# Kernel tuning notes

Measured on AMD Instinct MI355X. Metric: run time of the kernel, lower is better.

## Reference

```python
import jax, jax.numpy as jnp
import numpy as np

B, S, HID = 2, 2048, 2560
H, HKV, D = 8, 4, 256          # query heads, kv heads, head_dim
GROUPS = H // HKV
Q_SIZE, KV_SIZE = H * D, HKV * D
SLIDING_WINDOW = 512
SCALE = 256.0 ** -0.5          # query_pre_attn_scalar ** -0.5
EPS = 1e-6
ROPE_THETA = 10000.0


def setup_inputs() -> dict:
    key = jax.random.key(0)
    k1, k2, k3 = jax.random.split(key, 3)
    return {
        "hidden_states": jax.random.normal(k1, (B, S, HID), jnp.float32),
        "w_qkv": jax.random.normal(k2, (HID, Q_SIZE + 2 * KV_SIZE), jnp.float32) * (HID ** -0.5),
        "w_o": jax.random.normal(k3, (H * D, HID), jnp.float32) * ((H * D) ** -0.5),
        "q_norm_w": jnp.zeros((D,), jnp.float32),   # Gemma RMSNorm uses (1 + w)
        "k_norm_w": jnp.zeros((D,), jnp.float32),
        "positions": jnp.arange(S, dtype=jnp.int32),
    }


def _gemma_rms_norm(x, w, eps=EPS):
    # Gemma3RMSNorm: normalize in fp32, scale by (1 + w)
    xf = x.astype(jnp.float32)
    n = xf * jax.lax.rsqrt(jnp.mean(xf * xf, axis=-1, keepdims=True) + eps)
    return (n * (1.0 + w)).astype(x.dtype)


def _rope(q, k, positions):
    # q: [B,S,H,D], k: [B,S,HKV,D]; rotate_half RoPE, unsqueeze_dim=2 (head axis)
    half = D // 2
    inv_freq = 1.0 / (ROPE_THETA ** (jnp.arange(0, D, 2, dtype=jnp.float32) / D))  # [D/2]
    ang = positions.astype(jnp.float32)[:, None] * inv_freq[None, :]               # [S,D/2]
    emb = jnp.concatenate([ang, ang], axis=-1)                                     # [S,D]
    cos = jnp.cos(emb)[None, :, None, :]
    sin = jnp.sin(emb)[None, :, None, :]

    def rot(x):
        x1, x2 = x[..., :half], x[..., half:]
        return jnp.concatenate([-x2, x1], axis=-1)

    return q * cos + rot(q) * sin, k * cos + rot(k) * sin


def reference(hidden_states, w_qkv, w_o, q_norm_w, k_norm_w, positions):
    bsz, q_len, _ = hidden_states.shape
    qkv = jnp.einsum("bsh,hd->bsd", hidden_states, w_qkv)
    q, k, v = jnp.split(qkv, [Q_SIZE, Q_SIZE + KV_SIZE], axis=-1)
    Q = q.reshape(bsz, q_len, H, D)
    K = k.reshape(bsz, q_len, HKV, D)
    V = v.reshape(bsz, q_len, HKV, D)

    Q = _gemma_rms_norm(Q, q_norm_w)
    K = _gemma_rms_norm(K, k_norm_w)
    Q, K = _rope(Q, K, positions)

    # GQA: repeat kv heads to match query heads
    Kr = jnp.repeat(K, GROUPS, axis=2)  # [B,S,H,D]
    Vr = jnp.repeat(V, GROUPS, axis=2)

    scores = jnp.einsum("bqhd,bkhd->bhqk", Q, Kr) * SCALE  # [B,H,S,S]

    i = positions[:, None].astype(jnp.int32)
    j = positions[None, :].astype(jnp.int32)
    mask = (j <= i) & ((i - j) < SLIDING_WINDOW)           # causal + sliding window
    scores = jnp.where(mask[None, None, :, :], scores, jnp.float32(-1e30))

    probs = jax.nn.softmax(scores.astype(jnp.float32), axis=-1).astype(Q.dtype)
    out = jnp.einsum("bhqk,bkhd->bqhd", probs, Vr).reshape(bsz, q_len, H * D)
    return jnp.einsum("bsd,dh->bsh", out, w_o)
```

## Files before the change

### kernel.cpp

```cpp
#include <hip/hip_runtime.h>
#include <hip/hip_bf16.h>
#include <stdint.h>

#define QSCALE 0.09016844005555459f

typedef __attribute__((ext_vector_type(4))) float f32x4;
typedef __attribute__((ext_vector_type(8))) __bf16 bf16x8;
typedef __attribute__((ext_vector_type(8))) unsigned short ushort8;

static __device__ __forceinline__ float bf2f(unsigned short v) {
  union { unsigned u; float f; } x; x.u = ((unsigned)v) << 16; return x.f;
}
static __device__ __forceinline__ unsigned short f2bf(float f) {
  union { float f; unsigned u; } x; x.f = f;
  unsigned r = x.u + 0x7fffu + ((x.u >> 16) & 1u);
  return (unsigned short)(r >> 16);
}
static __device__ __forceinline__ void gload16(const void* g, void* l) {
  __builtin_amdgcn_global_load_lds((const __attribute__((address_space(1))) void*)g,
                                   (__attribute__((address_space(3))) void*)l, 16, 0, 0);
}
#define SBAR() __builtin_amdgcn_s_barrier()

__global__ __launch_bounds__(256) void k_rope_tab(const int* __restrict__ pos,
                                                  float* __restrict__ ct,
                                                  float* __restrict__ st) {
  int idx = blockIdx.x * 256 + threadIdx.x;
  int s = idx >> 7, j = idx & 127;
  float inv = exp2f((float)j * (-13.287712379549449f / 128.0f));
  float ang = (float)pos[s] * inv;
  float sv, cv;
  sincosf(ang, &sv, &cv);
  ct[idx] = cv; st[idx] = sv;
}

__global__ __launch_bounds__(256) void k_cvt_bf16(const float* __restrict__ in,
                                                  unsigned short* __restrict__ out, int n4) {
  int i = blockIdx.x * 256 + threadIdx.x;
  if (i >= n4) return;
  float4 v = ((const float4*)in)[i];
  ushort4 o; o.x = f2bf(v.x); o.y = f2bf(v.y); o.z = f2bf(v.z); o.w = f2bf(v.w);
  ((ushort4*)out)[i] = o;
}

__global__ __launch_bounds__(256) void k_transpose_w(const float* __restrict__ in,
                                                     unsigned short* __restrict__ out,
                                                     int R, int C) {
  __shared__ float tile[32][33];
  int c0 = blockIdx.x * 32, r0 = blockIdx.y * 32;
  int tx = threadIdx.x & 31, ty = threadIdx.x >> 5;
#pragma unroll
  for (int i = 0; i < 4; i++)
    tile[ty + 8*i][tx] = in[(size_t)(r0 + ty + 8*i) * C + c0 + tx];
  __syncthreads();
#pragma unroll
  for (int i = 0; i < 4; i++)
    out[(size_t)(c0 + ty + 8*i) * R + r0 + tx] = f2bf(tile[tx][ty + 8*i]);
}

template <bool F32OUT>
__global__ __launch_bounds__(512, 1) void k_gemm256(const unsigned short* __restrict__ A,
                                                    const unsigned short* __restrict__ Bt,
                                                    void* __restrict__ Cm,
                                                    int M, int N, int K) {
  __shared__ __align__(16) unsigned short ldsA[4][8192];
  __shared__ __align__(16) unsigned short ldsB[4][8192];
  const int nbn = N >> 8;
  int bid = blockIdx.x;
  int nwg = gridDim.x;
  if ((nwg & 7) == 0) {
    int cpx = nwg >> 3;
    bid = (bid & 7) * cpx + (bid >> 3);
  }
  const int bm = bid / nbn, bn = bid % nbn;
  const int tid = threadIdx.x;
  const int w = tid >> 6, l = tid & 63;
  const int wm = w >> 2, wn = w & 3;
  const int lr = l & 15, lk = l >> 4;
  const int nt = K >> 5;

  const int rL = tid >> 2;
  const int swc = ((tid & 3) ^ ((tid >> 3) & 3)) << 3;
  const unsigned short* Ag = A + (size_t)(bm * 256 + rL) * K + swc;
  const unsigned short* Bg = Bt + (size_t)(bn * 256 + rL) * K + swc;
  const int ldsoff = w * 512;
  const int wb = ((lk ^ ((lr >> 1) & 3)) << 3);
  const int arow0 = wm * 128 + lr;
  const int brow0 = wn * 64 + lr;

  f32x4 acc[8][4] = {};

#define STAGE_A(kt_, s_) do { \
    gload16(Ag + (size_t)(kt_) * 32,                    (char*)&ldsA[s_][ldsoff]); \
    gload16(Ag + (size_t)(kt_) * 32 + (size_t)128 * K,  (char*)&ldsA[s_][4096 + ldsoff]); } while (0)
#define STAGE_B(kt_, s_) do { \
    gload16(Bg + (size_t)(kt_) * 32,                    (char*)&ldsB[s_][ldsoff]); \
    gload16(Bg + (size_t)(kt_) * 32 + (size_t)128 * K,  (char*)&ldsB[s_][4096 + ldsoff]); } while (0)

#define KSTEP(kt_, S_, PF_, VMC_, TAILBAR_) do { \
    bf16x8 af[8], bf[4]; \
    _Pragma("unroll") \
    for (int i = 0; i < 8; ++i) \
      af[i] = *(const bf16x8*)&ldsA[S_][((arow0 + i * 16) << 5) + wb]; \
    _Pragma("unroll") \
    for (int j = 0; j < 4; ++j) \
      bf[j] = *(const bf16x8*)&ldsB[S_][((brow0 + j * 16) << 5) + wb]; \
    if (PF_) { STAGE_A((kt_) + 3, ((S_) + 3) & 3); STAGE_B((kt_) + 3, ((S_) + 3) & 3); } \
    __builtin_amdgcn_s_setprio(1); \
    _Pragma("unroll") \
    for (int i = 0; i < 8; ++i) \
      _Pragma("unroll") \
      for (int j = 0; j < 4; ++j) \
        acc[i][j] = __builtin_amdgcn_mfma_f32_16x16x32_bf16(af[i], bf[j], acc[i][j], 0, 0, 0); \
    __builtin_amdgcn_s_setprio(0); \
    if ((VMC_) == 8)      { asm volatile("s_waitcnt vmcnt(8)" ::: "memory"); } \
    else if ((VMC_) == 4) { asm volatile("s_waitcnt vmcnt(4)" ::: "memory"); } \
    else if ((VMC_) == 0) { asm volatile("s_waitcnt vmcnt(0)" ::: "memory"); } \
    if (TAILBAR_) SBAR(); \
  } while (0)

  STAGE_A(0, 0); STAGE_B(0, 0);
  STAGE_A(1, 1); STAGE_B(1, 1);
  STAGE_A(2, 2); STAGE_B(2, 2);
  asm volatile("s_waitcnt vmcnt(8)" ::: "memory");
  SBAR();

  const int ng = nt >> 2;
  for (int g = 0; g < ng - 1; ++g) {
    const int kt0 = g << 2;
    KSTEP(kt0 + 0, 0, true, 8, true);
    KSTEP(kt0 + 1, 1, true, 8, true);
    KSTEP(kt0 + 2, 2, true, 8, true);
    KSTEP(kt0 + 3, 3, true, 8, true);
  }
  {
    const int kt0 = nt - 4;
    KSTEP(kt0 + 0, 0, true, 8, true);
    KSTEP(kt0 + 1, 1, false, 4, true);
    KSTEP(kt0 + 2, 2, false, 0, true);
    KSTEP(kt0 + 3, 3, false, -1, false);
  }
#undef KSTEP
#undef STAGE_A
#undef STAGE_B

#pragma unroll
  for (int i = 0; i < 8; ++i)
#pragma unroll
    for (int j = 0; j < 4; ++j) {
      int row = bm * 256 + wm * 128 + i * 16 + lk * 4;
      int col = bn * 256 + wn * 64 + j * 16 + lr;
#pragma unroll
      for (int r = 0; r < 4; ++r) {
        if constexpr (F32OUT)
          ((float*)Cm)[(size_t)(row + r) * N + col] = acc[i][j][r];
        else
          ((unsigned short*)Cm)[(size_t)(row + r) * N + col] = f2bf(acc[i][j][r]);
      }
    }
}

__global__ __launch_bounds__(256) void k_norm_rope(
    const unsigned short* __restrict__ qkv,
    const float* __restrict__ qw, const float* __restrict__ kw,
    const float* __restrict__ ct, const float* __restrict__ st,
    unsigned short* __restrict__ Qh, unsigned short* __restrict__ Kh) {
  int gwid = (blockIdx.x * 256 + threadIdx.x) >> 6;
  int l = threadIdx.x & 63;
  int head = gwid % 12;
  int bs = gwid / 12;
  int b = bs >> 11, s = bs & 2047;
  bool isq = head < 8;
  int col = isq ? head * 256 : 2048 + (head - 8) * 256;
  const unsigned short* src = qkv + (size_t)bs * 4096 + col;
  int d0 = l * 4;
  ushort4 u = *(const ushort4*)(src + d0);
  float x0 = bf2f(u.x), x1 = bf2f(u.y), x2 = bf2f(u.z), x3 = bf2f(u.w);
  float ss = x0 * x0 + x1 * x1 + x2 * x2 + x3 * x3;
#pragma unroll
  for (int off = 32; off > 0; off >>= 1) ss += __shfl_xor(ss, off);
  float inv = rsqrtf(ss * (1.0f / 256.0f) + 1e-6f);
  const float* wv = isq ? qw : kw;
  float4 w4 = *(const float4*)(wv + d0);
  float y0 = x0 * inv * (1.0f + w4.x);
  float y1 = x1 * inv * (1.0f + w4.y);
  float y2 = x2 * inv * (1.0f + w4.z);
  float y3 = x3 * inv * (1.0f + w4.w);
  int fb = (l & 31) * 4;
  float4 c4 = *(const float4*)(ct + s * 128 + fb);
  float4 s4 = *(const float4*)(st + s * 128 + fb);
  float p0 = __shfl_xor(y0, 32), p1 = __shfl_xor(y1, 32);
  float p2 = __shfl_xor(y2, 32), p3 = __shfl_xor(y3, 32);
  float sg = (l < 32) ? -1.0f : 1.0f;
  float o0 = y0 * c4.x + sg * p0 * s4.x;
  float o1 = y1 * c4.y + sg * p1 * s4.y;
  float o2 = y2 * c4.z + sg * p2 * s4.z;
  float o3 = y3 * c4.w + sg * p3 * s4.w;
  if (isq) {
    o0 *= QSCALE; o1 *= QSCALE; o2 *= QSCALE; o3 *= QSCALE;
    unsigned short* dst = Qh + (((size_t)(b * 8 + head)) * 2048 + s) * 256 + d0;
    ushort4 o; o.x = f2bf(o0); o.y = f2bf(o1); o.z = f2bf(o2); o.w = f2bf(o3);
    *(ushort4*)dst = o;
  } else {
    int hk = head - 8;
    int ch = d0 >> 3;
    int dsw = ((ch ^ (s & 7)) << 3) | (d0 & 7);
    unsigned short* dst = Kh + (((size_t)(b * 4 + hk)) * 2048 + s) * 256 + dsw;
    ushort4 o; o.x = f2bf(o0); o.y = f2bf(o1); o.z = f2bf(o2); o.w = f2bf(o3);
    *(ushort4*)dst = o;
  }
}

__global__ __launch_bounds__(256) void k_vtrans(const unsigned short* __restrict__ qkv,
                                                unsigned short* __restrict__ VT) {
  __shared__ __align__(16) unsigned short tile[64][72];
  int bid = blockIdx.x;
  int dt = bid & 3, stile = (bid >> 2) & 31, hk = (bid >> 7) & 3, b = bid >> 9;
  int s0 = stile * 64, d0 = dt * 64;
  int t = threadIdx.x;
#pragma unroll
  for (int i = 0; i < 2; i++) {
    int flat = i * 256 + t;
    int sl = flat >> 3, dc = flat & 7;
    ushort8 v = *(const ushort8*)&qkv[(size_t)(b * 2048 + s0 + sl) * 4096 + 3072 + hk * 256 + d0 + dc * 8];
    *(ushort8*)&tile[sl][dc * 8] = v;
  }
  __syncthreads();
#pragma unroll
  for (int i = 0; i < 2; i++) {
    int flat = i * 256 + t;
    int dl = flat >> 3, sc = flat & 7;
    ushort8 v;
#pragma unroll
    for (int j = 0; j < 8; j++) v[j] = tile[sc * 8 + j][dl];
    int dg = d0 + dl;
    int chg = (s0 >> 3) + sc;
    int swc = chg ^ (dg & 7);
    *(ushort8*)&VT[((size_t)(b * 4 + hk) * 256 + dg) * 2048 + swc * 8] = v;
  }
}

__global__ __launch_bounds__(512) void k_attn(
    const unsigned short* __restrict__ Qh,
    const unsigned short* __restrict__ Kh,
    const unsigned short* __restrict__ VT,
    const int* __restrict__ pos,
    unsigned short* __restrict__ Ao) {
  __shared__ __align__(16) unsigned short Ks[2][64 * 256];
  __shared__ __align__(16) unsigned short Vs[2][256 * 64];
  __shared__ __align__(16) unsigned short Ps[8][16 * 72];
  int bid = blockIdx.x;
  int qt = bid & 31, hk = (bid >> 5) & 3, b = bid >> 7;
  int t = threadIdx.x, w = t >> 6, l = t & 63;
  int lr = l & 15, lk = l >> 4;
  int h = hk * 2 + (w >> 2);
  int q0 = qt * 64, qrow0 = q0 + (w & 3) * 16;
  const unsigned short* qbase = Qh + (((size_t)(b * 8 + h)) * 2048 + (qrow0 + lr)) * 256;
  bf16x8 qf[8];
#pragma unroll
  for (int c = 0; c < 8; c++) qf[c] = *(const bf16x8*)&qbase[c * 32 + lk * 8];
  int pq[4];
#pragma unroll
  for (int r = 0; r < 4; r++) pq[r] = pos[qrow0 + lk * 4 + r];
  float m[4], ll[4];
  f32x4 oacc[16];
  f32x4 zero4 = {0.f, 0.f, 0.f, 0.f};
#pragma unroll
  for (int r = 0; r < 4; r++) { m[r] = -1e30f; ll[r] = 0.0f; }
#pragma unroll
  for (int nd = 0; nd < 16; nd++) oacc[nd] = zero4;
  const char* Kbase = (const char*)(Kh + ((size_t)(b * 4 + hk)) * 2048 * 256);
  const char* Vbase = (const char*)(VT + ((size_t)(b * 4 + hk)) * 256 * 2048);
  int jlo = q0 - 511; if (jlo < 0) jlo = 0; jlo &= ~63;
  const int ntj = ((q0 + 64) - jlo) >> 6;

#define ASTAGE(tj_) do { \
    const int j0_ = jlo + (tj_) * 64; \
    char* kd_ = (char*)Ks[(tj_) & 1]; \
    char* vd_ = (char*)Vs[(tj_) & 1]; \
    _Pragma("unroll") \
    for (int i = 0; i < 4; i++) \
      gload16(Kbase + (size_t)j0_ * 512 + i * 8192 + t * 16, kd_ + i * 8192 + w * 1024); \
    _Pragma("unroll") \
    for (int i = 0; i < 4; i++) { \
      int off_ = i * 8192 + t * 16; \
      int d_ = off_ >> 7, rb_ = off_ & 127; \
      gload16(Vbase + (size_t)d_ * 4096 + j0_ * 2 + rb_, vd_ + i * 8192 + w * 1024); \
    } \
  } while (0)

  ASTAGE(0);
  for (int tj = 0; tj < ntj; ++tj) {
    const int j0 = jlo + tj * 64;
    const char* Kb = (const char*)Ks[tj & 1];
    const char* Vb = (const char*)Vs[tj & 1];
    if (tj + 1 < ntj) {
      ASTAGE(tj + 1);
      asm volatile("s_waitcnt vmcnt(8)" ::: "memory");
    } else {
      asm volatile("s_waitcnt vmcnt(0)" ::: "memory");
    }
    SBAR();
    f32x4 sacc[4];
#pragma unroll
    for (int n = 0; n < 4; n++) sacc[n] = zero4;
    __builtin_amdgcn_s_setprio(1);
#pragma unroll
    for (int n = 0; n < 4; n++) {
      int key = n * 16 + lr;
      int sw = (key & 7) << 4;
#pragma unroll
      for (int c = 0; c < 8; c++) {
        bf16x8 kf = *(const bf16x8*)(Kb + key * 512 + ((c * 64 + lk * 16) ^ sw));
        sacc[n] = __builtin_amdgcn_mfma_f32_16x16x32_bf16(qf[c], kf, sacc[n], 0, 0, 0);
      }
    }
    __builtin_amdgcn_s_setprio(0);
    int pk[4];
#pragma unroll
    for (int n = 0; n < 4; n++) pk[n] = pos[j0 + n * 16 + lr];
#pragma unroll
    for (int n = 0; n < 4; n++)
#pragma unroll
      for (int r = 0; r < 4; r++) {
        int dq = pq[r] - pk[n];
        if (!(dq >= 0 && dq < 512)) sacc[n][r] = -1e30f;
      }
    float tm[4], rs[4], mn[4], corr[4];
#pragma unroll
    for (int r = 0; r < 4; r++)
      tm[r] = fmaxf(fmaxf(sacc[0][r], sacc[1][r]), fmaxf(sacc[2][r], sacc[3][r]));
#pragma unroll
    for (int d = 1; d < 16; d <<= 1)
#pragma unroll
      for (int r = 0; r < 4; r++) tm[r] = fmaxf(tm[r], __shfl_xor(tm[r], d));
#pragma unroll
    for (int r = 0; r < 4; r++) {
      mn[r] = fmaxf(m[r], tm[r]);
      corr[r] = exp2f(m[r] - mn[r]);
      rs[r] = 0.f;
    }
#pragma unroll
    for (int n = 0; n < 4; n++)
#pragma unroll
      for (int r = 0; r < 4; r++) {
        float sv = sacc[n][r];
        float p = (sv > -1e29f) ? exp2f(sv - mn[r]) : 0.0f;
        sacc[n][r] = p;
        rs[r] += p;
      }
#pragma unroll
    for (int d = 1; d < 16; d <<= 1)
#pragma unroll
      for (int r = 0; r < 4; r++) rs[r] += __shfl_xor(rs[r], d);
#pragma unroll
    for (int r = 0; r < 4; r++) { ll[r] = ll[r] * corr[r] + rs[r]; m[r] = mn[r]; }
#pragma unroll
    for (int nd = 0; nd < 16; nd++)
#pragma unroll
      for (int r = 0; r < 4; r++) oacc[nd][r] *= corr[r];
#pragma unroll
    for (int n = 0; n < 4; n++)
#pragma unroll
      for (int r = 0; r < 4; r++)
        Ps[w][(lk * 4 + r) * 72 + n * 16 + lr] = f2bf(sacc[n][r]);
#pragma unroll
    for (int c2 = 0; c2 < 2; c2++) {
      bf16x8 pf = *(const bf16x8*)&Ps[w][lr * 72 + c2 * 32 + lk * 8];
      __builtin_amdgcn_s_setprio(1);
#pragma unroll
      for (int nd = 0; nd < 16; nd++) {
        int dr = nd * 16 + lr;
        bf16x8 vf = *(const bf16x8*)(Vb + dr * 128 + ((c2 * 64 + lk * 16) ^ ((dr & 7) << 4)));
        oacc[nd] = __builtin_amdgcn_mfma_f32_16x16x32_bf16(pf, vf, oacc[nd], 0, 0, 0);
      }
      __builtin_amdgcn_s_setprio(0);
    }
    SBAR();
  }
#undef ASTAGE
#pragma unroll
  for (int r = 0; r < 4; r++) ll[r] = 1.0f / ll[r];
#pragma unroll
  for (int nd = 0; nd < 16; nd++)
#pragma unroll
    for (int r = 0; r < 4; r++) {
      float v = oacc[nd][r] * ll[r];
      Ao[((size_t)(b * 2048 + qrow0 + lk * 4 + r)) * 2048 + h * 256 + nd * 16 + lr] = f2bf(v);
    }
}

extern "C" void kernel_launch(void* const* d_in, const int* in_sizes, int n_in,
                              void* d_out, int out_size, void* d_ws, size_t ws_size,
                              hipStream_t stream) {
  const float* hs   = (const float*)d_in[0];
  const float* wqkv = (const float*)d_in[1];
  const float* wo   = (const float*)d_in[2];
  const float* qnw  = (const float*)d_in[3];
  const float* knw  = (const float*)d_in[4];
  const int*   pos  = (const int*)d_in[5];
  float* out = (float*)d_out;

  char* base = (char*)d_ws;
  const size_t OFF_R0 = 0;
  const size_t OFF_R1 = 33554432;
  const size_t OFF_R2 = 54525952;
  const size_t OFF_R3 = 75497472;

  unsigned short* QKV = (unsigned short*)(base + OFF_R0);
  unsigned short* Ao  = (unsigned short*)(base + OFF_R0);
  unsigned short* WoT = (unsigned short*)(base + OFF_R0 + 16777216);
  unsigned short* Xb  = (unsigned short*)(base + OFF_R1);
  unsigned short* Qh  = (unsigned short*)(base + OFF_R1);
  unsigned short* WqT = (unsigned short*)(base + OFF_R2);
  unsigned short* Kh  = (unsigned short*)(base + OFF_R2);
  unsigned short* VT  = (unsigned short*)(base + OFF_R2 + 8388608);
  float* ct = (float*)(base + OFF_R3);
  float* st = (float*)(base + OFF_R3 + 1048576);

  k_rope_tab<<<1024, 256, 0, stream>>>(pos, ct, st);
  k_cvt_bf16<<<10240, 256, 0, stream>>>(hs, Xb, 2621440);
  k_transpose_w<<<dim3(128, 80), 256, 0, stream>>>(wqkv, WqT, 2560, 4096);
  k_gemm256<false><<<256, 512, 0, stream>>>(Xb, WqT, QKV, 4096, 4096, 2560);
  k_norm_rope<<<12288, 256, 0, stream>>>(QKV, qnw, knw, ct, st, Qh, Kh);
  k_vtrans<<<1024, 256, 0, stream>>>(QKV, VT);
  k_transpose_w<<<dim3(80, 64), 256, 0, stream>>>(wo, WoT, 2048, 2560);
  k_attn<<<256, 512, 0, stream>>>(Qh, Kh, VT, pos, Ao);
  k_gemm256<true><<<160, 512, 0, stream>>>(Ao, WoT, out, 4096, 2560, 2048);
}
```

Before: 232.4 us.

## Switch GEMM pipeline to double-buffered 64-wide K tiles

Replaces the 4-stage, 32-wide K pipeline in the bf16 GEMM with a 2-stage, 64-wide K tile. Each tile is split into two 32-wide halves, and the next tile is prefetched while the current one is computed. This halves the number of barriers and waitcnt points per K and issues larger load batches. The trade-off is a shallower prefetch distance and a full vmcnt(0) wait every tile, which can expose memory latency. The loop also assumes nt is even.

Result: slower. 247.0 us (+6.3%).

```diff
diff --git a/kernel.cpp b/kernel.cpp
--- a/kernel.cpp
+++ b/kernel.cpp
@@ -63,8 +63,8 @@
                                                     const unsigned short* __restrict__ Bt,
                                                     void* __restrict__ Cm,
                                                     int M, int N, int K) {
-  __shared__ __align__(16) unsigned short ldsA[4][8192];
-  __shared__ __align__(16) unsigned short ldsB[4][8192];
+  __shared__ __align__(16) unsigned short ldsA[2][16384];
+  __shared__ __align__(16) unsigned short ldsB[2][16384];
   const int nbn = N >> 8;
   int bid = blockIdx.x;
   int nwg = gridDim.x;
@@ -77,7 +77,7 @@
   const int w = tid >> 6, l = tid & 63;
   const int wm = w >> 2, wn = w & 3;
   const int lr = l & 15, lk = l >> 4;
-  const int nt = K >> 5;
+  const int nt = K >> 6;
 
   const int rL = tid >> 2;
   const int swc = ((tid & 3) ^ ((tid >> 3) & 3)) << 3;
@@ -90,22 +90,26 @@
 
   f32x4 acc[8][4] = {};
 
-#define STAGE_A(kt_, s_) do { \
-    gload16(Ag + (size_t)(kt_) * 32,                    (char*)&ldsA[s_][ldsoff]); \
-    gload16(Ag + (size_t)(kt_) * 32 + (size_t)128 * K,  (char*)&ldsA[s_][4096 + ldsoff]); } while (0)
-#define STAGE_B(kt_, s_) do { \
-    gload16(Bg + (size_t)(kt_) * 32,                    (char*)&ldsB[s_][ldsoff]); \
-    gload16(Bg + (size_t)(kt_) * 32 + (size_t)128 * K,  (char*)&ldsB[s_][4096 + ldsoff]); } while (0)
-
-#define KSTEP(kt_, S_, PF_, VMC_, TAILBAR_) do { \
+#define STAGE64(kt_, s_) do { \
+    const size_t kb_ = (size_t)(kt_) * 64; \
+    gload16(Ag + kb_,                         (char*)&ldsA[s_][ldsoff]); \
+    gload16(Ag + kb_ + (size_t)128 * K,       (char*)&ldsA[s_][4096 + ldsoff]); \
+    gload16(Ag + kb_ + 32,                    (char*)&ldsA[s_][8192 + ldsoff]); \
+    gload16(Ag + kb_ + 32 + (size_t)128 * K,  (char*)&ldsA[s_][12288 + ldsoff]); \
+    gload16(Bg + kb_,                         (char*)&ldsB[s_][ldsoff]); \
+    gload16(Bg + kb_ + (size_t)128 * K,       (char*)&ldsB[s_][4096 + ldsoff]); \
+    gload16(Bg + kb_ + 32,                    (char*)&ldsB[s_][8192 + ldsoff]); \
+    gload16(Bg + kb_ + 32 + (size_t)128 * K,  (char*)&ldsB[s_][12288 + ldsoff]); \
+  } while (0)
+
+#define HALF64(S_, KH_) do { \
     bf16x8 af[8], bf[4]; \
     _Pragma("unroll") \
     for (int i = 0; i < 8; ++i) \
-      af[i] = *(const bf16x8*)&ldsA[S_][((arow0 + i * 16) << 5) + wb]; \
+      af[i] = *(const bf16x8*)&ldsA[S_][(KH_) * 8192 + ((arow0 + i * 16) << 5) + wb]; \
     _Pragma("unroll") \
     for (int j = 0; j < 4; ++j) \
-      bf[j] = *(const bf16x8*)&ldsB[S_][((brow0 + j * 16) << 5) + wb]; \
-    if (PF_) { STAGE_A((kt_) + 3, ((S_) + 3) & 3); STAGE_B((kt_) + 3, ((S_) + 3) & 3); } \
+      bf[j] = *(const bf16x8*)&ldsB[S_][(KH_) * 8192 + ((brow0 + j * 16) << 5) + wb]; \
     __builtin_amdgcn_s_setprio(1); \
     _Pragma("unroll") \
     for (int i = 0; i < 8; ++i) \
@@ -113,36 +117,26 @@
       for (int j = 0; j < 4; ++j) \
         acc[i][j] = __builtin_amdgcn_mfma_f32_16x16x32_bf16(af[i], bf[j], acc[i][j], 0, 0, 0); \
     __builtin_amdgcn_s_setprio(0); \
-    if ((VMC_) == 8)      { asm volatile("s_waitcnt vmcnt(8)" ::: "memory"); } \
-    else if ((VMC_) == 4) { asm volatile("s_waitcnt vmcnt(4)" ::: "memory"); } \
-    else if ((VMC_) == 0) { asm volatile("s_waitcnt vmcnt(0)" ::: "memory"); } \
-    if (TAILBAR_) SBAR(); \
   } while (0)
 
-  STAGE_A(0, 0); STAGE_B(0, 0);
-  STAGE_A(1, 1); STAGE_B(1, 1);
-  STAGE_A(2, 2); STAGE_B(2, 2);
-  asm volatile("s_waitcnt vmcnt(8)" ::: "memory");
+#define TILE64(kt_, S_, PF_) do { \
+    if (PF_) STAGE64((kt_) + 1, 1 - (S_)); \
+    HALF64(S_, 0); \
+    HALF64(S_, 1); \
+    if (PF_) { asm volatile("s_waitcnt vmcnt(0)" ::: "memory"); SBAR(); } \
+  } while (0)
+
+  STAGE64(0, 0);
+  asm volatile("s_waitcnt vmcnt(0)" ::: "memory");
   SBAR();
 
-  const int ng = nt >> 2;
-  for (int g = 0; g < ng - 1; ++g) {
-    const int kt0 = g << 2;
-    KSTEP(kt0 + 0, 0, true, 8, true);
-    KSTEP(kt0 + 1, 1, true, 8, true);
-    KSTEP(kt0 + 2, 2, true, 8, true);
-    KSTEP(kt0 + 3, 3, true, 8, true);
-  }
-  {
-    const int kt0 = nt - 4;
-    KSTEP(kt0 + 0, 0, true, 8, true);
-    KSTEP(kt0 + 1, 1, false, 4, true);
-    KSTEP(kt0 + 2, 2, false, 0, true);
-    KSTEP(kt0 + 3, 3, false, -1, false);
-  }
-#undef KSTEP
-#undef STAGE_A
-#undef STAGE_B
+  for (int kt = 0; kt < nt; kt += 2) {
+    TILE64(kt, 0, true);
+    TILE64(kt + 1, 1, (kt + 2) < nt);
+  }
+#undef TILE64
+#undef HALF64
+#undef STAGE64
 
 #pragma unroll
   for (int i = 0; i < 8; ++i)
```
